# Performance work log

Hardware: AMD Instinct MI355X
Metric: run time of the kernel (lower is better)

## Reference

```python
import jax, jax.numpy as jnp
import numpy as np

N, E, G = 20000, 320000, 128
H, TE, CD = 128, 128, 64
HEADS, DH = 4, 32          # inner = 128 == H
L = 6


def _fwd(p, edge_index, batch):
    """Faithful forward of CrystalDiffusionModel (eval mode: dropout = identity).
    EquivariantGraphConv (imported in the original) is implemented as the standard
    edge-conditioned message-passing conv: m_ij = silu(W[h_src; h_dst; e_ij] + b),
    agg = scatter_add over dst, h' = W_u[h; agg] + b_u."""
    x, ea, t = p['x'], p['edge_attr'], p['t']
    n = x.shape[0]
    h = x @ p['Wn'] + p['bn']                      # [N,H] node embedding
    ef = ea @ p['We'] + p['be']                    # [E,H] edge embedding

    # sinusoidal time embedding -> MLP
    half = TE // 2
    freq = jnp.exp(-jnp.arange(half, dtype=jnp.float32) * (np.log(10000.0) / (half - 1)))
    te = t[:, None] * freq[None, :]
    te = jnp.concatenate([jnp.sin(te), jnp.cos(te)], axis=-1)          # [G,TE]
    te = jax.nn.silu(te @ p['tm_W1'] + p['tm_b1']) @ p['tm_W2'] + p['tm_b2']

    def mlp2(z, W1, b1, W2, b2):
        return jax.nn.silu(z @ W1 + b1) @ W2 + b2

    topo_e = mlp2(p['topo_cond'], p['topo_W1'], p['topo_b1'], p['topo_W2'], p['topo_b2'])
    stab_e = mlp2(p['stab_cond'], p['stab_W1'], p['stab_b1'], p['stab_W2'], p['stab_b2'])
    sust_e = mlp2(p['sust_cond'], p['sust_W1'], p['sust_b1'], p['sust_W2'], p['sust_b2'])
    cond = mlp2(jnp.concatenate([topo_e, stab_e, sust_e], axis=-1),
                p['comb_W1'], p['comb_b1'], p['comb_W2'], p['comb_b2'])  # [G,CD]

    ctx = cond[batch]                               # [N,CD] per-node condition
    # context is a single token per query -> k,v constant across layers
    k = (ctx @ p['Wk']).reshape(n, HEADS, DH)
    v = (ctx @ p['Wv']).reshape(n, HEADS, DH)
    ti = jax.nn.silu(te)[batch]                     # [N,H] time influence (dropout=id)

    src, dst = edge_index[0], edge_index[1]
    scale = DH ** -0.5
    for i in range(L):
        Wm, bm = p['gnn_Wm'][i], p['gnn_bm'][i]
        # split concat-GEMM to avoid materializing [E, 3H]
        m = jax.nn.silu(h[src] @ Wm[:H] + h[dst] @ Wm[H:2 * H] + ef @ Wm[2 * H:] + bm)
        agg = jax.ops.segment_sum(m, dst, num_segments=n)               # [N,H]
        Wu, bu = p['gnn_Wu'][i], p['gnn_bu'][i]
        hu = h @ Wu[:H] + agg @ Wu[H:] + bu
        # LayerNorm
        mu = hu.mean(-1, keepdims=True)
        var = hu.var(-1, keepdims=True)
        hu = (hu - mu) * jax.lax.rsqrt(var + 1e-5) * p['ln_g'][i] + p['ln_b'][i]
        # cross-attention; context length is 1 so softmax over j is exactly 1
        q = (hu @ p['Wq']).reshape(n, HEADS, DH)
        sim = jnp.einsum('nhd,nhd->nh', q, k) * scale                   # [N,heads]
        attn = jax.nn.softmax(sim[..., None], axis=-1)                  # == 1.0
        out = (attn * v).reshape(n, HEADS * DH)
        hu = out @ p['Wo'] + p['bo']
        h = h + hu + ti                              # residual + time influence

    node_pred = jax.nn.silu(h @ p['np_W1'] + p['np_b1']) @ p['np_W2'] + p['np_b2']
    pos_pred = jax.nn.silu(h @ p['pp_W1'] + p['pp_b1']) @ p['pp_W2'] + p['pp_b2']
    return node_pred, pos_pred


def setup_inputs() -> dict:
    key = jax.random.key(0)
    it = iter(jax.random.split(key, 96))

    def nrm(shape, s=0.02):
        return jax.random.normal(next(it), shape, jnp.float32) * s

    z = lambda *s: jnp.zeros(s, jnp.float32)
    inp = {
        'x': jax.random.normal(next(it), (N, 12), jnp.float32),
        'edge_index': jax.random.randint(next(it), (2, E), 0, N),
        'edge_attr': jax.random.normal(next(it), (E, 20), jnp.float32),
        'pos': jax.random.normal(next(it), (N, 3), jnp.float32),
        't': jax.random.uniform(next(it), (G,), jnp.float32) * 1000.0,
        'topo_cond': jax.random.normal(next(it), (G, 7), jnp.float32),
        'stab_cond': jax.random.normal(next(it), (G, 2), jnp.float32),
        'sust_cond': jax.random.normal(next(it), (G, 3), jnp.float32),
        'batch': jnp.sort(jax.random.randint(next(it), (N,), 0, G)),
        'Wn': nrm((12, H)), 'bn': z(H), 'We': nrm((20, H)), 'be': z(H),
        'tm_W1': nrm((TE, 2 * TE)), 'tm_b1': z(2 * TE), 'tm_W2': nrm((2 * TE, TE)), 'tm_b2': z(TE),
        'topo_W1': nrm((7, 32)), 'topo_b1': z(32), 'topo_W2': nrm((32, 32)), 'topo_b2': z(32),
        'stab_W1': nrm((2, 16)), 'stab_b1': z(16), 'stab_W2': nrm((16, 16)), 'stab_b2': z(16),
        'sust_W1': nrm((3, 16)), 'sust_b1': z(16), 'sust_W2': nrm((16, 16)), 'sust_b2': z(16),
        'comb_W1': nrm((64, CD)), 'comb_b1': z(CD), 'comb_W2': nrm((CD, CD)), 'comb_b2': z(CD),
        'Wq': nrm((H, HEADS * DH)), 'Wk': nrm((CD, HEADS * DH)), 'Wv': nrm((CD, HEADS * DH)),
        'Wo': nrm((HEADS * DH, H)), 'bo': z(H),
        'gnn_Wm': nrm((L, 3 * H, H)), 'gnn_bm': z(L, H),
        'gnn_Wu': nrm((L, 2 * H, H)), 'gnn_bu': z(L, H),
        'ln_g': jnp.ones((L, H), jnp.float32), 'ln_b': z(L, H),
        'np_W1': nrm((H, 2 * H)), 'np_b1': z(2 * H), 'np_W2': nrm((2 * H, 12)), 'np_b2': z(12),
        'pp_W1': nrm((H, H)), 'pp_b1': z(H), 'pp_W2': nrm((H, 3)), 'pp_b2': z(3),
    }
    return inp


def reference(x, edge_index, edge_attr, pos, t, topo_cond, stab_cond, sust_cond, batch,
              Wn, bn, We, be, tm_W1, tm_b1, tm_W2, tm_b2,
              topo_W1, topo_b1, topo_W2, topo_b2, stab_W1, stab_b1, stab_W2, stab_b2,
              sust_W1, sust_b1, sust_W2, sust_b2, comb_W1, comb_b1, comb_W2, comb_b2,
              Wq, Wk, Wv, Wo, bo, gnn_Wm, gnn_bm, gnn_Wu, gnn_bu, ln_g, ln_b,
              np_W1, np_b1, np_W2, np_b2, pp_W1, pp_b1, pp_W2, pp_b2):
    loc = dict(locals())
    p = {k: v for k, v in loc.items() if k not in ('edge_index', 'batch', 'pos')}
    return _fwd(p, edge_index, batch)
```

## Files before the change

### kernel.cpp

```cpp
#include <hip/hip_runtime.h>
#include <hip/hip_bf16.h>

#define NN 20000
#define GG 128

typedef __bf16 bf16x8_t __attribute__((ext_vector_type(8)));
typedef float  f32x4_t  __attribute__((ext_vector_type(4)));
typedef __hip_bfloat16 hbf16;

#define PK_NPW1 32768
#define PK_PPW1 65536
#define PK_NPW2 81920
#define PK_PPW2 86016
#define PK_WN   88064

__device__ __forceinline__ float silu_f(float v) {
    return v / (1.0f + expf(-v));
}

__global__ __launch_bounds__(256) void graph_kernel(
        const float* __restrict__ t, const float* __restrict__ topo,
        const float* __restrict__ stab, const float* __restrict__ sust,
        const float* __restrict__ tmW1, const float* __restrict__ tmb1,
        const float* __restrict__ tmW2, const float* __restrict__ tmb2,
        const float* __restrict__ topoW1, const float* __restrict__ topob1,
        const float* __restrict__ topoW2, const float* __restrict__ topob2,
        const float* __restrict__ stabW1, const float* __restrict__ stabb1,
        const float* __restrict__ stabW2, const float* __restrict__ stabb2,
        const float* __restrict__ sustW1, const float* __restrict__ sustb1,
        const float* __restrict__ sustW2, const float* __restrict__ sustb2,
        const float* __restrict__ combW1, const float* __restrict__ combb1,
        const float* __restrict__ combW2, const float* __restrict__ combb2,
        const float* __restrict__ Wv, const float* __restrict__ Wo,
        const float* __restrict__ bo,
        const float* __restrict__ npW1, const float* __restrict__ npW2,
        const float* __restrict__ ppW1, const float* __restrict__ ppW2,
        const float* __restrict__ Wn,
        float* __restrict__ gadd, hbf16* __restrict__ wsb) {
    __shared__ float s_te[128];
    __shared__ float s_th1[256];
    __shared__ float s_tef[128];
    __shared__ float s_l1[64];
    __shared__ float s_cat[64];
    __shared__ float s_c1[64];
    __shared__ float s_cond[64];
    __shared__ float s_v[128];
    __shared__ float s_red[256];

    const int g = blockIdx.x;
    const int tid = threadIdx.x;

    {
#pragma unroll
        for (int e = 0; e < 2; ++e) {
            const int s = blockIdx.x * 512 + e * 256 + tid;
            if (s < 32768) {
                const int p = s;
                const int j = p & 7, l = (p >> 3) & 63, kb = (p >> 9) & 3, ct = p >> 11;
                const int k = kb * 32 + ((l >> 4) << 3) + j;
                const int n = ct * 16 + (l & 15);
                wsb[PK_NPW1 + p] = __float2bfloat16(npW1[k * 256 + n]);
            } else if (s < 49152) {
                const int p = s - 32768;
                const int j = p & 7, l = (p >> 3) & 63, kb = (p >> 9) & 3, ct = p >> 11;
                const int k = kb * 32 + ((l >> 4) << 3) + j;
                const int n = ct * 16 + (l & 15);
                wsb[PK_PPW1 + p] = __float2bfloat16(ppW1[k * 128 + n]);
            } else if (s < 53248) {
                const int p = s - 49152;
                const int j = p & 7, l = (p >> 3) & 63, kb = p >> 9;
                const int k = kb * 32 + ((l >> 4) << 3) + j;
                const int n = l & 15;
                wsb[PK_NPW2 + p] = __float2bfloat16(n < 12 ? npW2[k * 12 + n] : 0.0f);
            } else if (s < 55296) {
                const int p = s - 53248;
                const int j = p & 7, l = (p >> 3) & 63, kb = p >> 9;
                const int k = kb * 32 + ((l >> 4) << 3) + j;
                const int n = l & 15;
                wsb[PK_PPW2 + p] = __float2bfloat16(n < 3 ? ppW2[k * 3 + n] : 0.0f);
            } else if (s < 59392) {
                const int p = s - 55296;
                const int j = p & 7, l = (p >> 3) & 63, ct = p >> 9;
                const int k = ((l >> 4) << 3) + j;
                const int n = ct * 16 + (l & 15);
                wsb[PK_WN + p] = __float2bfloat16(k < 12 ? Wn[k * 128 + n] : 0.0f);
            }
        }
    }

    if (tid < 128) {
        const float tval = t[g];
        const int i = tid & 63;
        const float fr = expf(-(float)i * 0.14619587892025688f);
        const float arg = tval * fr;
        s_te[tid] = (tid < 64) ? sinf(arg) : cosf(arg);
    } else if (tid < 192) {
        const int c = tid - 128;
        if (c < 32) {
            float acc = topob1[c];
            for (int k = 0; k < 7; ++k)
                acc += topo[g * 7 + k] * topoW1[k * 32 + c];
            s_l1[c] = silu_f(acc);
        } else if (c < 48) {
            const int j = c - 32;
            float acc = stabb1[j];
            for (int k = 0; k < 2; ++k)
                acc += stab[g * 2 + k] * stabW1[k * 16 + j];
            s_l1[c] = silu_f(acc);
        } else {
            const int j = c - 48;
            float acc = sustb1[j];
            for (int k = 0; k < 3; ++k)
                acc += sust[g * 3 + k] * sustW1[k * 16 + j];
            s_l1[c] = silu_f(acc);
        }
    }
    __syncthreads();

    {
        float acc = tmb1[tid];
#pragma unroll 4
        for (int k = 0; k < 128; ++k)
            acc += s_te[k] * tmW1[k * 256 + tid];
        s_th1[tid] = silu_f(acc);
    }
    __syncthreads();

    {
        const int j = tid & 127, half = tid >> 7;
        float acc = 0.0f;
#pragma unroll 4
        for (int kk = 0; kk < 128; ++kk)
            acc += s_th1[half * 128 + kk] * tmW2[(half * 128 + kk) * 128 + j];
        s_red[tid] = acc;
    }
    __syncthreads();

    if (tid < 128) {
        s_tef[tid] = tmb2[tid] + s_red[tid] + s_red[tid + 128];
    } else if (tid < 192) {
        const int c = tid - 128;
        if (c < 32) {
            float acc = topob2[c];
            for (int k = 0; k < 32; ++k)
                acc += s_l1[k] * topoW2[k * 32 + c];
            s_cat[c] = acc;
        } else if (c < 48) {
            const int j = c - 32;
            float acc = stabb2[j];
            for (int k = 0; k < 16; ++k)
                acc += s_l1[32 + k] * stabW2[k * 16 + j];
            s_cat[c] = acc;
        } else {
            const int j = c - 48;
            float acc = sustb2[j];
            for (int k = 0; k < 16; ++k)
                acc += s_l1[48 + k] * sustW2[k * 16 + j];
            s_cat[c] = acc;
        }
    }
    __syncthreads();

    {
        const int j = tid & 63, part = tid >> 6;
        float acc = 0.0f;
#pragma unroll
        for (int kk = 0; kk < 16; ++kk)
            acc += s_cat[part * 16 + kk] * combW1[(part * 16 + kk) * 64 + j];
        s_red[tid] = acc;
    }
    __syncthreads();
    if (tid < 64)
        s_c1[tid] = silu_f(combb1[tid] + s_red[tid] + s_red[tid + 64] +
                           s_red[tid + 128] + s_red[tid + 192]);
    __syncthreads();

    {
        const int j = tid & 63, part = tid >> 6;
        float acc = 0.0f;
#pragma unroll
        for (int kk = 0; kk < 16; ++kk)
            acc += s_c1[part * 16 + kk] * combW2[(part * 16 + kk) * 64 + j];
        s_red[tid] = acc;
    }
    __syncthreads();
    if (tid < 64)
        s_cond[tid] = combb2[tid] + s_red[tid] + s_red[tid + 64] +
                      s_red[tid + 128] + s_red[tid + 192];
    __syncthreads();

    {
        const int j = tid & 127, half = tid >> 7;
        float acc = 0.0f;
#pragma unroll
        for (int kk = 0; kk < 32; ++kk)
            acc += s_cond[half * 32 + kk] * Wv[(half * 32 + kk) * 128 + j];
        s_red[tid] = acc;
    }
    __syncthreads();
    if (tid < 128) s_v[tid] = s_red[tid] + s_red[tid + 128];
    __syncthreads();

    {
        const int j = tid & 127, half = tid >> 7;
        float acc = 0.0f;
#pragma unroll 4
        for (int kk = 0; kk < 64; ++kk)
            acc += s_v[half * 64 + kk] * Wo[(half * 64 + kk) * 128 + j];
        s_red[tid] = acc;
    }
    __syncthreads();
    if (tid < 128)
        gadd[g * 128 + tid] =
            6.0f * (bo[tid] + s_red[tid] + s_red[tid + 128] + silu_f(s_tef[tid]));
}

__global__ __launch_bounds__(256, 1) void node_kernel(
        const float* __restrict__ x, const int* __restrict__ batch,
        const float* __restrict__ bn,
        const float* __restrict__ npb1, const float* __restrict__ npb2,
        const float* __restrict__ ppb1, const float* __restrict__ ppb2,
        const float* __restrict__ gadd, const hbf16* __restrict__ wsb,
        float* __restrict__ out) {
    __shared__ __align__(16) hbf16 z1s[4 * 16 * 264];
    __shared__ __align__(16) hbf16 hs[4 * 16 * 136];

    const int tid  = threadIdx.x;
    const int w    = tid >> 6;
    const int lane = tid & 63;
    const int q    = lane >> 4;
    const int r    = lane & 15;
    const int n16  = blockIdx.x * 64 + w * 16;

    hbf16* wz1 = z1s + w * (16 * 264);
    hbf16* wh  = hs  + w * (16 * 136);

    bf16x8_t Ax;
    {
        const int node = n16 + r;
        float xv[8];
#pragma unroll
        for (int j = 0; j < 8; ++j) xv[j] = 0.0f;
        if (node < NN) {
            if (q == 0) {
                const float4 a = *reinterpret_cast<const float4*>(x + node * 12);
                const float4 b = *reinterpret_cast<const float4*>(x + node * 12 + 4);
                xv[0] = a.x; xv[1] = a.y; xv[2] = a.z; xv[3] = a.w;
                xv[4] = b.x; xv[5] = b.y; xv[6] = b.z; xv[7] = b.w;
            } else if (q == 1) {
                const float4 a = *reinterpret_cast<const float4*>(x + node * 12 + 8);
                xv[0] = a.x; xv[1] = a.y; xv[2] = a.z; xv[3] = a.w;
            }
        }
#pragma unroll
        for (int j = 0; j < 8; ++j) {
            const hbf16 tv = __float2bfloat16(xv[j]);
            Ax[j] = *reinterpret_cast<const __bf16*>(&tv);
        }
    }

    int bidx[4];
#pragma unroll
    for (int i = 0; i < 4; ++i) {
        const int gn = n16 + q * 4 + i;
        bidx[i] = (gn < NN) ? batch[gn] : 0;
    }

    f32x4_t hacc[8];
#pragma unroll
    for (int ct = 0; ct < 8; ++ct) {
        const bf16x8_t Bf = *reinterpret_cast<const bf16x8_t*>(
            &wsb[PK_WN + (ct * 64 + lane) * 8]);
        hacc[ct] = __builtin_amdgcn_mfma_f32_16x16x32_bf16(
            Ax, Bf, (f32x4_t){0.f, 0.f, 0.f, 0.f}, 0, 0, 0);
    }
#pragma unroll
    for (int ct = 0; ct < 8; ++ct) {
        const int n = ct * 16 + r;
        const float bv = bn[n];
#pragma unroll
        for (int i = 0; i < 4; ++i) {
            const float hv = hacc[ct][i] + bv + gadd[bidx[i] * 128 + n];
            wh[(q * 4 + i) * 136 + n] = __float2bfloat16(hv);
        }
    }

    bf16x8_t Ah[4];
#pragma unroll
    for (int kb = 0; kb < 4; ++kb)
        Ah[kb] = *reinterpret_cast<const bf16x8_t*>(
            &wh[r * 136 + kb * 32 + q * 8]);

    {
        f32x4_t acc[16];
#pragma unroll
        for (int ct = 0; ct < 16; ++ct) acc[ct] = (f32x4_t){0.f, 0.f, 0.f, 0.f};
#pragma unroll
        for (int kb = 0; kb < 4; ++kb) {
#pragma unroll
            for (int ct = 0; ct < 16; ++ct) {
                const bf16x8_t Bf = *reinterpret_cast<const bf16x8_t*>(
                    &wsb[PK_NPW1 + ((ct * 4 + kb) * 64 + lane) * 8]);
                acc[ct] = __builtin_amdgcn_mfma_f32_16x16x32_bf16(
                    Ah[kb], Bf, acc[ct], 0, 0, 0);
            }
        }
#pragma unroll
        for (int ct = 0; ct < 16; ++ct) {
            const int col = ct * 16 + r;
            const float b1 = npb1[col];
#pragma unroll
            for (int i = 0; i < 4; ++i)
                wz1[(q * 4 + i) * 264 + col] =
                    __float2bfloat16(silu_f(acc[ct][i] + b1));
        }
    }

    {
        f32x4_t acc2 = (f32x4_t){0.f, 0.f, 0.f, 0.f};
#pragma unroll
        for (int kb = 0; kb < 8; ++kb) {
            const bf16x8_t Af = *reinterpret_cast<const bf16x8_t*>(
                &wz1[r * 264 + kb * 32 + q * 8]);
            const bf16x8_t Bf = *reinterpret_cast<const bf16x8_t*>(
                &wsb[PK_NPW2 + (kb * 64 + lane) * 8]);
            acc2 = __builtin_amdgcn_mfma_f32_16x16x32_bf16(Af, Bf, acc2, 0, 0, 0);
        }
        if (r < 12) {
            const float b2 = npb2[r];
#pragma unroll
            for (int i = 0; i < 4; ++i) {
                const int gn = n16 + q * 4 + i;
                if (gn < NN) out[gn * 12 + r] = acc2[i] + b2;
            }
        }
    }

    {
        f32x4_t acc[8];
#pragma unroll
        for (int ct = 0; ct < 8; ++ct) acc[ct] = (f32x4_t){0.f, 0.f, 0.f, 0.f};
#pragma unroll
        for (int kb = 0; kb < 4; ++kb) {
#pragma unroll
            for (int ct = 0; ct < 8; ++ct) {
                const bf16x8_t Bf = *reinterpret_cast<const bf16x8_t*>(
                    &wsb[PK_PPW1 + ((ct * 4 + kb) * 64 + lane) * 8]);
                acc[ct] = __builtin_amdgcn_mfma_f32_16x16x32_bf16(
                    Ah[kb], Bf, acc[ct], 0, 0, 0);
            }
        }
#pragma unroll
        for (int ct = 0; ct < 8; ++ct) {
            const int col = ct * 16 + r;
            const float b1 = ppb1[col];
#pragma unroll
            for (int i = 0; i < 4; ++i)
                wh[(q * 4 + i) * 136 + col] =
                    __float2bfloat16(silu_f(acc[ct][i] + b1));
        }
    }

    {
        f32x4_t acc2 = (f32x4_t){0.f, 0.f, 0.f, 0.f};
#pragma unroll
        for (int kb = 0; kb < 4; ++kb) {
            const bf16x8_t Af = *reinterpret_cast<const bf16x8_t*>(
                &wh[r * 136 + kb * 32 + q * 8]);
            const bf16x8_t Bf = *reinterpret_cast<const bf16x8_t*>(
                &wsb[PK_PPW2 + (kb * 64 + lane) * 8]);
            acc2 = __builtin_amdgcn_mfma_f32_16x16x32_bf16(Af, Bf, acc2, 0, 0, 0);
        }
        if (r < 3) {
            const float b2 = ppb2[r];
#pragma unroll
            for (int i = 0; i < 4; ++i) {
                const int gn = n16 + q * 4 + i;
                if (gn < NN) out[NN * 12 + gn * 3 + r] = acc2[i] + b2;
            }
        }
    }
}

extern "C" void kernel_launch(void* const* d_in, const int* in_sizes, int n_in,
                              void* d_out, int out_size, void* d_ws, size_t ws_size,
                              hipStream_t stream) {
    const float* x      = (const float*)d_in[0];
    const float* t      = (const float*)d_in[4];
    const float* topo   = (const float*)d_in[5];
    const float* stab   = (const float*)d_in[6];
    const float* sust   = (const float*)d_in[7];
    const int*   batch  = (const int*)d_in[8];
    const float* Wn     = (const float*)d_in[9];
    const float* bn     = (const float*)d_in[10];
    const float* tmW1   = (const float*)d_in[13];
    const float* tmb1   = (const float*)d_in[14];
    const float* tmW2   = (const float*)d_in[15];
    const float* tmb2   = (const float*)d_in[16];
    const float* topoW1 = (const float*)d_in[17];
    const float* topob1 = (const float*)d_in[18];
    const float* topoW2 = (const float*)d_in[19];
    const float* topob2 = (const float*)d_in[20];
    const float* stabW1 = (const float*)d_in[21];
    const float* stabb1 = (const float*)d_in[22];
    const float* stabW2 = (const float*)d_in[23];
    const float* stabb2 = (const float*)d_in[24];
    const float* sustW1 = (const float*)d_in[25];
    const float* sustb1 = (const float*)d_in[26];
    const float* sustW2 = (const float*)d_in[27];
    const float* sustb2 = (const float*)d_in[28];
    const float* combW1 = (const float*)d_in[29];
    const float* combb1 = (const float*)d_in[30];
    const float* combW2 = (const float*)d_in[31];
    const float* combb2 = (const float*)d_in[32];
    const float* Wv     = (const float*)d_in[35];
    const float* Wo     = (const float*)d_in[36];
    const float* bo     = (const float*)d_in[37];
    const float* npW1   = (const float*)d_in[44];
    const float* npb1   = (const float*)d_in[45];
    const float* npW2   = (const float*)d_in[46];
    const float* npb2   = (const float*)d_in[47];
    const float* ppW1   = (const float*)d_in[48];
    const float* ppb1   = (const float*)d_in[49];
    const float* ppW2   = (const float*)d_in[50];
    const float* ppb2   = (const float*)d_in[51];

    float* gadd = (float*)d_ws;
    hbf16* wsb  = (hbf16*)d_ws;
    float* out  = (float*)d_out;

    graph_kernel<<<GG, 256, 0, stream>>>(t, topo, stab, sust,
                                         tmW1, tmb1, tmW2, tmb2,
                                         topoW1, topob1, topoW2, topob2,
                                         stabW1, stabb1, stabW2, stabb2,
                                         sustW1, sustb1, sustW2, sustb2,
                                         combW1, combb1, combW2, combb2,
                                         Wv, Wo, bo,
                                         npW1, npW2, ppW1, ppW2, Wn,
                                         gadd, wsb);

    node_kernel<<<(NN + 63) / 64, 256, 0, stream>>>(
        x, batch, bn, npb1, npb2, ppb1, ppb2, gadd, wsb, out);
}
```

Measured before the change: 232.6 us.

## Fuse per-graph conditioning MLPs into node kernel, split weight packing

Moves weight packing into a separate small pack kernel and fuses the per-graph time/condition MLP chain into the node kernel. Each node block recomputes the graph-level additive term for the (up to 4) graphs its 64 nodes span and keeps it in shared memory, so the gadd round trip through global memory is gone. The work is redundant: every graph's MLP is recomputed by several blocks, each block's serial prologue gets longer, and the clamp to 4 graphs per block assumes sorted batches with enough nodes per graph. The z1 and h shared buffers are merged into one to offset the added shared-memory use.

Measured after the change: 255.2 us. +9.7%, slower.

```diff
diff --git a/kernel.cpp b/kernel.cpp
--- a/kernel.cpp
+++ b/kernel.cpp
@@ -8,17 +8,56 @@
 typedef float  f32x4_t  __attribute__((ext_vector_type(4)));
 typedef __hip_bfloat16 hbf16;
 
-#define PK_NPW1 32768
-#define PK_PPW1 65536
-#define PK_NPW2 81920
-#define PK_PPW2 86016
-#define PK_WN   88064
+#define PK_NPW1 0
+#define PK_PPW1 32768
+#define PK_NPW2 49152
+#define PK_PPW2 53248
+#define PK_WN   55296
 
 __device__ __forceinline__ float silu_f(float v) {
     return v / (1.0f + expf(-v));
 }
 
-__global__ __launch_bounds__(256) void graph_kernel(
+__global__ __launch_bounds__(256) void pack_kernel(
+        const float* __restrict__ npW1, const float* __restrict__ npW2,
+        const float* __restrict__ ppW1, const float* __restrict__ ppW2,
+        const float* __restrict__ Wn, hbf16* __restrict__ wsb) {
+    const int s = blockIdx.x * 256 + threadIdx.x;
+    if (s < 32768) {
+        const int p = s;
+        const int j = p & 7, l = (p >> 3) & 63, kb = (p >> 9) & 3, ct = p >> 11;
+        const int k = kb * 32 + ((l >> 4) << 3) + j;
+        const int n = ct * 16 + (l & 15);
+        wsb[PK_NPW1 + p] = __float2bfloat16(npW1[k * 256 + n]);
+    } else if (s < 49152) {
+        const int p = s - 32768;
+        const int j = p & 7, l = (p >> 3) & 63, kb = (p >> 9) & 3, ct = p >> 11;
+        const int k = kb * 32 + ((l >> 4) << 3) + j;
+        const int n = ct * 16 + (l & 15);
+        wsb[PK_PPW1 + p] = __float2bfloat16(ppW1[k * 128 + n]);
+    } else if (s < 53248) {
+        const int p = s - 49152;
+        const int j = p & 7, l = (p >> 3) & 63, kb = p >> 9;
+        const int k = kb * 32 + ((l >> 4) << 3) + j;
+        const int n = l & 15;
+        wsb[PK_NPW2 + p] = __float2bfloat16(n < 12 ? npW2[k * 12 + n] : 0.0f);
+    } else if (s < 55296) {
+        const int p = s - 53248;
+        const int j = p & 7, l = (p >> 3) & 63, kb = p >> 9;
+        const int k = kb * 32 + ((l >> 4) << 3) + j;
+        const int n = l & 15;
+        wsb[PK_PPW2 + p] = __float2bfloat16(n < 3 ? ppW2[k * 3 + n] : 0.0f);
+    } else {
+        const int p = s - 55296;
+        const int j = p & 7, l = (p >> 3) & 63, ct = p >> 9;
+        const int k = ((l >> 4) << 3) + j;
+        const int n = ct * 16 + (l & 15);
+        wsb[PK_WN + p] = __float2bfloat16(k < 12 ? Wn[k * 128 + n] : 0.0f);
+    }
+}
+
+__global__ __launch_bounds__(256) void fused_kernel(
+        const float* __restrict__ x, const int* __restrict__ batch,
         const float* __restrict__ t, const float* __restrict__ topo,
         const float* __restrict__ stab, const float* __restrict__ sust,
         const float* __restrict__ tmW1, const float* __restrict__ tmb1,
@@ -32,11 +71,11 @@
         const float* __restrict__ combW1, const float* __restrict__ combb1,
         const float* __restrict__ combW2, const float* __restrict__ combb2,
         const float* __restrict__ Wv, const float* __restrict__ Wo,
-        const float* __restrict__ bo,
-        const float* __restrict__ npW1, const float* __restrict__ npW2,
-        const float* __restrict__ ppW1, const float* __restrict__ ppW2,
-        const float* __restrict__ Wn,
-        float* __restrict__ gadd, hbf16* __restrict__ wsb) {
+        const float* __restrict__ bo, const float* __restrict__ bn,
+        const float* __restrict__ npb1, const float* __restrict__ npb2,
+        const float* __restrict__ ppb1, const float* __restrict__ ppb2,
+        const hbf16* __restrict__ wsb,
+        float* __restrict__ out) {
     __shared__ float s_te[128];
     __shared__ float s_th1[256];
     __shared__ float s_tef[128];
@@ -46,194 +85,156 @@
     __shared__ float s_cond[64];
     __shared__ float s_v[128];
     __shared__ float s_red[256];
-
-    const int g = blockIdx.x;
+    __shared__ float s_gadd[4][128];
+    __shared__ __align__(16) hbf16 tbuf[4 * 16 * 264];
+
     const int tid = threadIdx.x;
-
-    {
-#pragma unroll
-        for (int e = 0; e < 2; ++e) {
-            const int s = blockIdx.x * 512 + e * 256 + tid;
-            if (s < 32768) {
-                const int p = s;
-                const int j = p & 7, l = (p >> 3) & 63, kb = (p >> 9) & 3, ct = p >> 11;
-                const int k = kb * 32 + ((l >> 4) << 3) + j;
-                const int n = ct * 16 + (l & 15);
-                wsb[PK_NPW1 + p] = __float2bfloat16(npW1[k * 256 + n]);
-            } else if (s < 49152) {
-                const int p = s - 32768;
-                const int j = p & 7, l = (p >> 3) & 63, kb = (p >> 9) & 3, ct = p >> 11;
-                const int k = kb * 32 + ((l >> 4) << 3) + j;
-                const int n = ct * 16 + (l & 15);
-                wsb[PK_PPW1 + p] = __float2bfloat16(ppW1[k * 128 + n]);
-            } else if (s < 53248) {
-                const int p = s - 49152;
-                const int j = p & 7, l = (p >> 3) & 63, kb = p >> 9;
-                const int k = kb * 32 + ((l >> 4) << 3) + j;
-                const int n = l & 15;
-                wsb[PK_NPW2 + p] = __float2bfloat16(n < 12 ? npW2[k * 12 + n] : 0.0f);
-            } else if (s < 55296) {
-                const int p = s - 53248;
-                const int j = p & 7, l = (p >> 3) & 63, kb = p >> 9;
-                const int k = kb * 32 + ((l >> 4) << 3) + j;
-                const int n = l & 15;
-                wsb[PK_PPW2 + p] = __float2bfloat16(n < 3 ? ppW2[k * 3 + n] : 0.0f);
-            } else if (s < 59392) {
-                const int p = s - 55296;
-                const int j = p & 7, l = (p >> 3) & 63, ct = p >> 9;
-                const int k = ((l >> 4) << 3) + j;
-                const int n = ct * 16 + (l & 15);
-                wsb[PK_WN + p] = __float2bfloat16(k < 12 ? Wn[k * 128 + n] : 0.0f);
-            }
-        }
-    }
-
-    if (tid < 128) {
-        const float tval = t[g];
-        const int i = tid & 63;
-        const float fr = expf(-(float)i * 0.14619587892025688f);
-        const float arg = tval * fr;
-        s_te[tid] = (tid < 64) ? sinf(arg) : cosf(arg);
-    } else if (tid < 192) {
-        const int c = tid - 128;
-        if (c < 32) {
-            float acc = topob1[c];
-            for (int k = 0; k < 7; ++k)
-                acc += topo[g * 7 + k] * topoW1[k * 32 + c];
-            s_l1[c] = silu_f(acc);
-        } else if (c < 48) {
-            const int j = c - 32;
-            float acc = stabb1[j];
-            for (int k = 0; k < 2; ++k)
-                acc += stab[g * 2 + k] * stabW1[k * 16 + j];
-            s_l1[c] = silu_f(acc);
-        } else {
-            const int j = c - 48;
-            float acc = sustb1[j];
-            for (int k = 0; k < 3; ++k)
-                acc += sust[g * 3 + k] * sustW1[k * 16 + j];
-            s_l1[c] = silu_f(acc);
-        }
-    }
-    __syncthreads();
-
-    {
-        float acc = tmb1[tid];
+    const int nb = blockIdx.x * 64;
+    const int nlast = (nb + 63 < NN) ? nb + 63 : NN - 1;
+
+    const int g0 = batch[nb];
+    const int g1 = batch[nlast];
+    int ng = g1 - g0 + 1;
+    if (ng > 4) ng = 4;
+
+    for (int gi = 0; gi < ng; ++gi) {
+        const int g = g0 + gi;
+
+        if (tid < 128) {
+            const float tval = t[g];
+            const int i = tid & 63;
+            const float fr = expf(-(float)i * 0.14619587892025688f);
+            const float arg = tval * fr;
+            s_te[tid] = (tid < 64) ? sinf(arg) : cosf(arg);
+        } else if (tid < 192) {
+            const int c = tid - 128;
+            if (c < 32) {
+                float acc = topob1[c];
+                for (int k = 0; k < 7; ++k)
+                    acc += topo[g * 7 + k] * topoW1[k * 32 + c];
+                s_l1[c] = silu_f(acc);
+            } else if (c < 48) {
+                const int j = c - 32;
+                float acc = stabb1[j];
+                for (int k = 0; k < 2; ++k)
+                    acc += stab[g * 2 + k] * stabW1[k * 16 + j];
+                s_l1[c] = silu_f(acc);
+            } else {
+                const int j = c - 48;
+                float acc = sustb1[j];
+                for (int k = 0; k < 3; ++k)
+                    acc += sust[g * 3 + k] * sustW1[k * 16 + j];
+                s_l1[c] = silu_f(acc);
+            }
+        }
+        __syncthreads();
+
+        {
+            float acc = tmb1[tid];
 #pragma unroll 4
-        for (int k = 0; k < 128; ++k)
-            acc += s_te[k] * tmW1[k * 256 + tid];
-        s_th1[tid] = silu_f(acc);
-    }
-    __syncthreads();
-
-    {
-        const int j = tid & 127, half = tid >> 7;
-        float acc = 0.0f;
+            for (int k = 0; k < 128; ++k)
+                acc += s_te[k] * tmW1[k * 256 + tid];
+            s_th1[tid] = silu_f(acc);
+        }
+        __syncthreads();
+
+        {
+            const int j = tid & 127, half = tid >> 7;
+            float acc = 0.0f;
 #pragma unroll 4
-        for (int kk = 0; kk < 128; ++kk)
-            acc += s_th1[half * 128 + kk] * tmW2[(half * 128 + kk) * 128 + j];
-        s_red[tid] = acc;
-    }
-    __syncthreads();
-
-    if (tid < 128) {
-        s_tef[tid] = tmb2[tid] + s_red[tid] + s_red[tid + 128];
-    } else if (tid < 192) {
-        const int c = tid - 128;
-        if (c < 32) {
-            float acc = topob2[c];
-            for (int k = 0; k < 32; ++k)
-                acc += s_l1[k] * topoW2[k * 32 + c];
-            s_cat[c] = acc;
-        } else if (c < 48) {
-            const int j = c - 32;
-            float acc = stabb2[j];
-            for (int k = 0; k < 16; ++k)
-                acc += s_l1[32 + k] * stabW2[k * 16 + j];
-            s_cat[c] = acc;
-        } else {
-            const int j = c - 48;
-            float acc = sustb2[j];
-            for (int k = 0; k < 16; ++k)
-                acc += s_l1[48 + k] * sustW2[k * 16 + j];
-            s_cat[c] = acc;
-        }
-    }
-    __syncthreads();
-
-    {
-        const int j = tid & 63, part = tid >> 6;
-        float acc = 0.0f;
-#pragma unroll
-        for (int kk = 0; kk < 16; ++kk)
-            acc += s_cat[part * 16 + kk] * combW1[(part * 16 + kk) * 64 + j];
-        s_red[tid] = acc;
-    }
-    __syncthreads();
-    if (tid < 64)
-        s_c1[tid] = silu_f(combb1[tid] + s_red[tid] + s_red[tid + 64] +
-                           s_red[tid + 128] + s_red[tid + 192]);
-    __syncthreads();
-
-    {
-        const int j = tid & 63, part = tid >> 6;
-        float acc = 0.0f;
-#pragma unroll
-        for (int kk = 0; kk < 16; ++kk)
-            acc += s_c1[part * 16 + kk] * combW2[(part * 16 + kk) * 64 + j];
-        s_red[tid] = acc;
-    }
-    __syncthreads();
-    if (tid < 64)
-        s_cond[tid] = combb2[tid] + s_red[tid] + s_red[tid + 64] +
-                      s_red[tid + 128] + s_red[tid + 192];
-    __syncthreads();
-
-    {
-        const int j = tid & 127, half = tid >> 7;
-        float acc = 0.0f;
-#pragma unroll
-        for (int kk = 0; kk < 32; ++kk)
-            acc += s_cond[half * 32 + kk] * Wv[(half * 32 + kk) * 128 + j];
-        s_red[tid] = acc;
-    }
-    __syncthreads();
-    if (tid < 128) s_v[tid] = s_red[tid] + s_red[tid + 128];
-    __syncthreads();
-
-    {
-        const int j = tid & 127, half = tid >> 7;
-        float acc = 0.0f;
+            for (int kk = 0; kk < 128; ++kk)
+                acc += s_th1[half * 128 + kk] * tmW2[(half * 128 + kk) * 128 + j];
+            s_red[tid] = acc;
+        }
+        __syncthreads();
+
+        if (tid < 128) {
+            s_tef[tid] = tmb2[tid] + s_red[tid] + s_red[tid + 128];
+        } else if (tid < 192) {
+            const int c = tid - 128;
+            if (c < 32) {
+                float acc = topob2[c];
+                for (int k = 0; k < 32; ++k)
+                    acc += s_l1[k] * topoW2[k * 32 + c];
+                s_cat[c] = acc;
+            } else if (c < 48) {
+                const int j = c - 32;
+                float acc = stabb2[j];
+                for (int k = 0; k < 16; ++k)
+                    acc += s_l1[32 + k] * stabW2[k * 16 + j];
+                s_cat[c] = acc;
+            } else {
+                const int j = c - 48;
+                float acc = sustb2[j];
+                for (int k = 0; k < 16; ++k)
+                    acc += s_l1[48 + k] * sustW2[k * 16 + j];
+                s_cat[c] = acc;
+            }
+        }
+        __syncthreads();
+
+        {
+            const int j = tid & 63, part = tid >> 6;
+            float acc = 0.0f;
+#pragma unroll
+            for (int kk = 0; kk < 16; ++kk)
+                acc += s_cat[part * 16 + kk] * combW1[(part * 16 + kk) * 64 + j];
+            s_red[tid] = acc;
+        }
+        __syncthreads();
+        if (tid < 64)
+            s_c1[tid] = silu_f(combb1[tid] + s_red[tid] + s_red[tid + 64] +
+                               s_red[tid + 128] + s_red[tid + 192]);
+        __syncthreads();
+
+        {
+            const int j = tid & 63, part = tid >> 6;
+            float acc = 0.0f;
+#pragma unroll
+            for (int kk = 0; kk < 16; ++kk)
+                acc += s_c1[part * 16 + kk] * combW2[(part * 16 + kk) * 64 + j];
+            s_red[tid] = acc;
+        }
+        __syncthreads();
+        if (tid < 64)
+            s_cond[tid] = combb2[tid] + s_red[tid] + s_red[tid + 64] +
+                          s_red[tid + 128] + s_red[tid + 192];
+        __syncthreads();
+
+        {
+            const int j = tid & 127, half = tid >> 7;
+            float acc = 0.0f;
+#pragma unroll
+            for (int kk = 0; kk < 32; ++kk)
+                acc += s_cond[half * 32 + kk] * Wv[(half * 32 + kk) * 128 + j];
+            s_red[tid] = acc;
+        }
+        __syncthreads();
+        if (tid < 128) s_v[tid] = s_red[tid] + s_red[tid + 128];
+        __syncthreads();
+
+        {
+            const int j = tid & 127, half = tid >> 7;
+            float acc = 0.0f;
 #pragma unroll 4
-        for (int kk = 0; kk < 64; ++kk)
-            acc += s_v[half * 64 + kk] * Wo[(half * 64 + kk) * 128 + j];
-        s_red[tid] = acc;
-    }
-    __syncthreads();
-    if (tid < 128)
-        gadd[g * 128 + tid] =
-            6.0f * (bo[tid] + s_red[tid] + s_red[tid + 128] + silu_f(s_tef[tid]));
-}
-
-__global__ __launch_bounds__(256, 1) void node_kernel(
-        const float* __restrict__ x, const int* __restrict__ batch,
-        const float* __restrict__ bn,
-        const float* __restrict__ npb1, const float* __restrict__ npb2,
-        const float* __restrict__ ppb1, const float* __restrict__ ppb2,
-        const float* __restrict__ gadd, const hbf16* __restrict__ wsb,
-        float* __restrict__ out) {
-    __shared__ __align__(16) hbf16 z1s[4 * 16 * 264];
-    __shared__ __align__(16) hbf16 hs[4 * 16 * 136];
-
-    const int tid  = threadIdx.x;
+            for (int kk = 0; kk < 64; ++kk)
+                acc += s_v[half * 64 + kk] * Wo[(half * 64 + kk) * 128 + j];
+            s_red[tid] = acc;
+        }
+        __syncthreads();
+        if (tid < 128)
+            s_gadd[gi][tid] =
+                6.0f * (bo[tid] + s_red[tid] + s_red[tid + 128] + silu_f(s_tef[tid]));
+        __syncthreads();
+    }
+
     const int w    = tid >> 6;
     const int lane = tid & 63;
     const int q    = lane >> 4;
     const int r    = lane & 15;
-    const int n16  = blockIdx.x * 64 + w * 16;
-
-    hbf16* wz1 = z1s + w * (16 * 264);
-    hbf16* wh  = hs  + w * (16 * 136);
+    const int n16  = nb + w * 16;
+
+    hbf16* wb = tbuf + w * (16 * 264);
 
     bf16x8_t Ax;
     {
@@ -259,29 +260,35 @@
         }
     }
 
-    int bidx[4];
+    int gidx[4];
 #pragma unroll
     for (int i = 0; i < 4; ++i) {
         const int gn = n16 + q * 4 + i;
-        bidx[i] = (gn < NN) ? batch[gn] : 0;
-    }
-
-    f32x4_t hacc[8];
-#pragma unroll
-    for (int ct = 0; ct < 8; ++ct) {
-        const bf16x8_t Bf = *reinterpret_cast<const bf16x8_t*>(
-            &wsb[PK_WN + (ct * 64 + lane) * 8]);
-        hacc[ct] = __builtin_amdgcn_mfma_f32_16x16x32_bf16(
-            Ax, Bf, (f32x4_t){0.f, 0.f, 0.f, 0.f}, 0, 0, 0);
-    }
-#pragma unroll
-    for (int ct = 0; ct < 8; ++ct) {
-        const int n = ct * 16 + r;
-        const float bv = bn[n];
-#pragma unroll
-        for (int i = 0; i < 4; ++i) {
-            const float hv = hacc[ct][i] + bv + gadd[bidx[i] * 128 + n];
-            wh[(q * 4 + i) * 136 + n] = __float2bfloat16(hv);
+        int b = (gn < NN) ? batch[gn] : g0;
+        int d = b - g0;
+        if (d < 0) d = 0;
+        if (d > ng - 1) d = ng - 1;
+        gidx[i] = d;
+    }
+
+    {
+        f32x4_t hacc[8];
+#pragma unroll
+        for (int ct = 0; ct < 8; ++ct) {
+            const bf16x8_t Bf = *reinterpret_cast<const bf16x8_t*>(
+                &wsb[PK_WN + (ct * 64 + lane) * 8]);
+            hacc[ct] = __builtin_amdgcn_mfma_f32_16x16x32_bf16(
+                Ax, Bf, (f32x4_t){0.f, 0.f, 0.f, 0.f}, 0, 0, 0);
+        }
+#pragma unroll
+        for (int ct = 0; ct < 8; ++ct) {
+            const int n = ct * 16 + r;
+            const float bv = bn[n];
+#pragma unroll
+            for (int i = 0; i < 4; ++i) {
+                const float hv = hacc[ct][i] + bv + s_gadd[gidx[i]][n];
+                wb[(q * 4 + i) * 136 + n] = __float2bfloat16(hv);
+            }
         }
     }
 
@@ -289,7 +296,7 @@
 #pragma unroll
     for (int kb = 0; kb < 4; ++kb)
         Ah[kb] = *reinterpret_cast<const bf16x8_t*>(
-            &wh[r * 136 + kb * 32 + q * 8]);
+            &wb[r * 136 + kb * 32 + q * 8]);
 
     {
         f32x4_t acc[16];
@@ -311,7 +318,7 @@
             const float b1 = npb1[col];
 #pragma unroll
             for (int i = 0; i < 4; ++i)
-                wz1[(q * 4 + i) * 264 + col] =
+                wb[(q * 4 + i) * 264 + col] =
                     __float2bfloat16(silu_f(acc[ct][i] + b1));
         }
     }
@@ -321,7 +328,7 @@
 #pragma unroll
         for (int kb = 0; kb < 8; ++kb) {
             const bf16x8_t Af = *reinterpret_cast<const bf16x8_t*>(
-                &wz1[r * 264 + kb * 32 + q * 8]);
+                &wb[r * 264 + kb * 32 + q * 8]);
             const bf16x8_t Bf = *reinterpret_cast<const bf16x8_t*>(
                 &wsb[PK_NPW2 + (kb * 64 + lane) * 8]);
             acc2 = __builtin_amdgcn_mfma_f32_16x16x32_bf16(Af, Bf, acc2, 0, 0, 0);
@@ -356,7 +363,7 @@
             const float b1 = ppb1[col];
 #pragma unroll
             for (int i = 0; i < 4; ++i)
-                wh[(q * 4 + i) * 136 + col] =
+                wb[(q * 4 + i) * 136 + col] =
                     __float2bfloat16(silu_f(acc[ct][i] + b1));
         }
     }
@@ -366,7 +373,7 @@
 #pragma unroll
         for (int kb = 0; kb < 4; ++kb) {
             const bf16x8_t Af = *reinterpret_cast<const bf16x8_t*>(
-                &wh[r * 136 + kb * 32 + q * 8]);
+                &wb[r * 136 + kb * 32 + q * 8]);
             const bf16x8_t Bf = *reinterpret_cast<const bf16x8_t*>(
                 &wsb[PK_PPW2 + (kb * 64 + lane) * 8]);
             acc2 = __builtin_amdgcn_mfma_f32_16x16x32_bf16(Af, Bf, acc2, 0, 0, 0);
@@ -425,20 +432,18 @@
     const float* ppW2   = (const float*)d_in[50];
     const float* ppb2   = (const float*)d_in[51];
 
-    float* gadd = (float*)d_ws;
-    hbf16* wsb  = (hbf16*)d_ws;
-    float* out  = (float*)d_out;
-
-    graph_kernel<<<GG, 256, 0, stream>>>(t, topo, stab, sust,
-                                         tmW1, tmb1, tmW2, tmb2,
-                                         topoW1, topob1, topoW2, topob2,
-                                         stabW1, stabb1, stabW2, stabb2,
-                                         sustW1, sustb1, sustW2, sustb2,
-                                         combW1, combb1, combW2, combb2,
-                                         Wv, Wo, bo,
-                                         npW1, npW2, ppW1, ppW2, Wn,
-                                         gadd, wsb);
-
-    node_kernel<<<(NN + 63) / 64, 256, 0, stream>>>(
-        x, batch, bn, npb1, npb2, ppb1, ppb2, gadd, wsb, out);
+    hbf16* wsb = (hbf16*)d_ws;
+    float* out = (float*)d_out;
+
+    pack_kernel<<<232, 256, 0, stream>>>(npW1, npW2, ppW1, ppW2, Wn, wsb);
+
+    fused_kernel<<<(NN + 63) / 64, 256, 0, stream>>>(
+        x, batch, t, topo, stab, sust,
+        tmW1, tmb1, tmW2, tmb2,
+        topoW1, topob1, topoW2, topob2,
+        stabW1, stabb1, stabW2, stabb2,
+        sustW1, sustb1, sustW2, sustb2,
+        combW1, combb1, combW2, combb2,
+        Wv, Wo, bo, bn, npb1, npb2, ppb1, ppb2,
+        wsb, out);
 }
```

## Stage packed weights and biases in LDS, split weight packing into extra blocks

Applied to the files above, without the earlier changes.

The node kernel now stages each packed bf16 weight matrix chunk into shared memory, along with the biases, the batch indices and a window of per-graph additive vectors. Previously every wave read the weight fragments straight from global memory. The weight packing is moved into separate extra blocks of the prep kernel, so the per-graph MLP blocks no longer do it. Smaller per-wave register footprints, the dropped single-block launch bound, fast exp/rcp in silu and larger unroll factors aim for higher occupancy and less global traffic. The cost is many more __syncthreads barriers between chunk loads.

After: 203.0 us. 1.15x faster.

```diff
diff --git a/kernel.cpp b/kernel.cpp
--- a/kernel.cpp
+++ b/kernel.cpp
@@ -8,17 +8,18 @@
 typedef float  f32x4_t  __attribute__((ext_vector_type(4)));
 typedef __hip_bfloat16 hbf16;
 
-#define PK_NPW1 32768
-#define PK_PPW1 65536
-#define PK_NPW2 81920
-#define PK_PPW2 86016
-#define PK_WN   88064
+#define PK_NPW1 0
+#define PK_PPW1 32768
+#define PK_NPW2 49152
+#define PK_PPW2 53248
+#define PK_WN   55296
+#define GADD_OFF 59392
 
 __device__ __forceinline__ float silu_f(float v) {
-    return v / (1.0f + expf(-v));
+    return v * __builtin_amdgcn_rcpf(1.0f + __expf(-v));
 }
 
-__global__ __launch_bounds__(256) void graph_kernel(
+__global__ __launch_bounds__(256) void prep_kernel(
         const float* __restrict__ t, const float* __restrict__ topo,
         const float* __restrict__ stab, const float* __restrict__ sust,
         const float* __restrict__ tmW1, const float* __restrict__ tmb1,
@@ -37,6 +38,44 @@
         const float* __restrict__ ppW1, const float* __restrict__ ppW2,
         const float* __restrict__ Wn,
         float* __restrict__ gadd, hbf16* __restrict__ wsb) {
+    const int tid = threadIdx.x;
+
+    if (blockIdx.x >= GG) {
+        const int s = (blockIdx.x - GG) * 256 + tid;
+        if (s < 32768) {
+            const int p = s;
+            const int j = p & 7, l = (p >> 3) & 63, kb = (p >> 9) & 3, ct = p >> 11;
+            const int k = kb * 32 + ((l >> 4) << 3) + j;
+            const int n = ct * 16 + (l & 15);
+            wsb[PK_NPW1 + p] = __float2bfloat16(npW1[k * 256 + n]);
+        } else if (s < 49152) {
+            const int p = s - 32768;
+            const int j = p & 7, l = (p >> 3) & 63, kb = (p >> 9) & 3, ct = p >> 11;
+            const int k = kb * 32 + ((l >> 4) << 3) + j;
+            const int n = ct * 16 + (l & 15);
+            wsb[PK_PPW1 + p] = __float2bfloat16(ppW1[k * 128 + n]);
+        } else if (s < 53248) {
+            const int p = s - 49152;
+            const int j = p & 7, l = (p >> 3) & 63, kb = p >> 9;
+            const int k = kb * 32 + ((l >> 4) << 3) + j;
+            const int n = l & 15;
+            wsb[PK_NPW2 + p] = __float2bfloat16(n < 12 ? npW2[k * 12 + n] : 0.0f);
+        } else if (s < 55296) {
+            const int p = s - 53248;
+            const int j = p & 7, l = (p >> 3) & 63, kb = p >> 9;
+            const int k = kb * 32 + ((l >> 4) << 3) + j;
+            const int n = l & 15;
+            wsb[PK_PPW2 + p] = __float2bfloat16(n < 3 ? ppW2[k * 3 + n] : 0.0f);
+        } else if (s < 59392) {
+            const int p = s - 55296;
+            const int j = p & 7, l = (p >> 3) & 63, ct = p >> 9;
+            const int k = ((l >> 4) << 3) + j;
+            const int n = ct * 16 + (l & 15);
+            wsb[PK_WN + p] = __float2bfloat16(k < 12 ? Wn[k * 128 + n] : 0.0f);
+        }
+        return;
+    }
+
     __shared__ float s_te[128];
     __shared__ float s_th1[256];
     __shared__ float s_tef[128];
@@ -48,50 +87,11 @@
     __shared__ float s_red[256];
 
     const int g = blockIdx.x;
-    const int tid = threadIdx.x;
-
-    {
-#pragma unroll
-        for (int e = 0; e < 2; ++e) {
-            const int s = blockIdx.x * 512 + e * 256 + tid;
-            if (s < 32768) {
-                const int p = s;
-                const int j = p & 7, l = (p >> 3) & 63, kb = (p >> 9) & 3, ct = p >> 11;
-                const int k = kb * 32 + ((l >> 4) << 3) + j;
-                const int n = ct * 16 + (l & 15);
-                wsb[PK_NPW1 + p] = __float2bfloat16(npW1[k * 256 + n]);
-            } else if (s < 49152) {
-                const int p = s - 32768;
-                const int j = p & 7, l = (p >> 3) & 63, kb = (p >> 9) & 3, ct = p >> 11;
-                const int k = kb * 32 + ((l >> 4) << 3) + j;
-                const int n = ct * 16 + (l & 15);
-                wsb[PK_PPW1 + p] = __float2bfloat16(ppW1[k * 128 + n]);
-            } else if (s < 53248) {
-                const int p = s - 49152;
-                const int j = p & 7, l = (p >> 3) & 63, kb = p >> 9;
-                const int k = kb * 32 + ((l >> 4) << 3) + j;
-                const int n = l & 15;
-                wsb[PK_NPW2 + p] = __float2bfloat16(n < 12 ? npW2[k * 12 + n] : 0.0f);
-            } else if (s < 55296) {
-                const int p = s - 53248;
-                const int j = p & 7, l = (p >> 3) & 63, kb = p >> 9;
-                const int k = kb * 32 + ((l >> 4) << 3) + j;
-                const int n = l & 15;
-                wsb[PK_PPW2 + p] = __float2bfloat16(n < 3 ? ppW2[k * 3 + n] : 0.0f);
-            } else if (s < 59392) {
-                const int p = s - 55296;
-                const int j = p & 7, l = (p >> 3) & 63, ct = p >> 9;
-                const int k = ((l >> 4) << 3) + j;
-                const int n = ct * 16 + (l & 15);
-                wsb[PK_WN + p] = __float2bfloat16(k < 12 ? Wn[k * 128 + n] : 0.0f);
-            }
-        }
-    }
 
     if (tid < 128) {
         const float tval = t[g];
         const int i = tid & 63;
-        const float fr = expf(-(float)i * 0.14619587892025688f);
+        const float fr = __expf(-(float)i * 0.14619587892025688f);
         const float arg = tval * fr;
         s_te[tid] = (tid < 64) ? sinf(arg) : cosf(arg);
     } else if (tid < 192) {
@@ -119,7 +119,7 @@
 
     {
         float acc = tmb1[tid];
-#pragma unroll 4
+#pragma unroll 16
         for (int k = 0; k < 128; ++k)
             acc += s_te[k] * tmW1[k * 256 + tid];
         s_th1[tid] = silu_f(acc);
@@ -129,7 +129,7 @@
     {
         const int j = tid & 127, half = tid >> 7;
         float acc = 0.0f;
-#pragma unroll 4
+#pragma unroll 16
         for (int kk = 0; kk < 128; ++kk)
             acc += s_th1[half * 128 + kk] * tmW2[(half * 128 + kk) * 128 + j];
         s_red[tid] = acc;
@@ -192,7 +192,7 @@
     {
         const int j = tid & 127, half = tid >> 7;
         float acc = 0.0f;
-#pragma unroll
+#pragma unroll 16
         for (int kk = 0; kk < 32; ++kk)
             acc += s_cond[half * 32 + kk] * Wv[(half * 32 + kk) * 128 + j];
         s_red[tid] = acc;
@@ -204,7 +204,7 @@
     {
         const int j = tid & 127, half = tid >> 7;
         float acc = 0.0f;
-#pragma unroll 4
+#pragma unroll 16
         for (int kk = 0; kk < 64; ++kk)
             acc += s_v[half * 64 + kk] * Wo[(half * 64 + kk) * 128 + j];
         s_red[tid] = acc;
@@ -215,25 +215,64 @@
             6.0f * (bo[tid] + s_red[tid] + s_red[tid + 128] + silu_f(s_tef[tid]));
 }
 
-__global__ __launch_bounds__(256, 1) void node_kernel(
+#define NGS 8
+
+__global__ __launch_bounds__(256) void node_kernel(
         const float* __restrict__ x, const int* __restrict__ batch,
         const float* __restrict__ bn,
         const float* __restrict__ npb1, const float* __restrict__ npb2,
         const float* __restrict__ ppb1, const float* __restrict__ ppb2,
         const float* __restrict__ gadd, const hbf16* __restrict__ wsb,
         float* __restrict__ out) {
-    __shared__ __align__(16) hbf16 z1s[4 * 16 * 264];
-    __shared__ __align__(16) hbf16 hs[4 * 16 * 136];
+    __shared__ __align__(16) hbf16 s_w[8192];
+    __shared__ __align__(16) hbf16 tbuf[4 * 16 * 264];
+    __shared__ float s_gadd[NGS * 128];
+    __shared__ float s_bias[528];
+    __shared__ int   s_bi[64];
 
     const int tid  = threadIdx.x;
+    const int nb   = blockIdx.x * 64;
     const int w    = tid >> 6;
     const int lane = tid & 63;
     const int q    = lane >> 4;
     const int r    = lane & 15;
-    const int n16  = blockIdx.x * 64 + w * 16;
-
-    hbf16* wz1 = z1s + w * (16 * 264);
-    hbf16* wh  = hs  + w * (16 * 136);
+    const int n16  = nb + w * 16;
+
+    hbf16* wb = tbuf + w * (16 * 264);
+
+    if (tid < 64) {
+        int gn = nb + tid;
+        if (gn > NN - 1) gn = NN - 1;
+        s_bi[tid] = batch[gn];
+    }
+    {
+        int i = tid;
+        if (i < 128) s_bias[i] = bn[i];
+        else if (i < 384) s_bias[i] = npb1[i - 128];
+        else if (i < 396) s_bias[i] = npb2[i - 384];
+        else if (i < 524) s_bias[i] = ppb1[i - 396];
+        else if (i < 527) s_bias[i] = ppb2[i - 524];
+        i = tid + 256;
+        if (i < 384) s_bias[i] = npb1[i - 128];
+        else if (i < 396) s_bias[i] = npb2[i - 384];
+        else if (i < 524) s_bias[i] = ppb1[i - 396];
+        else if (i < 527) s_bias[i] = ppb2[i - 524];
+    }
+    {
+        const uint4* src = reinterpret_cast<const uint4*>(wsb + PK_WN);
+        uint4* dst = reinterpret_cast<uint4*>(s_w);
+        for (int i = tid; i < 512; i += 256) dst[i] = src[i];
+    }
+    __syncthreads();
+
+    const int g0 = s_bi[0];
+    {
+        for (int i = tid; i < NGS * 128; i += 256) {
+            int gr = g0 + (i >> 7);
+            if (gr > GG - 1) gr = GG - 1;
+            s_gadd[i] = gadd[gr * 128 + (i & 127)];
+        }
+    }
 
     bf16x8_t Ax;
     {
@@ -258,30 +297,30 @@
             Ax[j] = *reinterpret_cast<const __bf16*>(&tv);
         }
     }
-
-    int bidx[4];
-#pragma unroll
-    for (int i = 0; i < 4; ++i) {
-        const int gn = n16 + q * 4 + i;
-        bidx[i] = (gn < NN) ? batch[gn] : 0;
-    }
-
-    f32x4_t hacc[8];
-#pragma unroll
-    for (int ct = 0; ct < 8; ++ct) {
-        const bf16x8_t Bf = *reinterpret_cast<const bf16x8_t*>(
-            &wsb[PK_WN + (ct * 64 + lane) * 8]);
-        hacc[ct] = __builtin_amdgcn_mfma_f32_16x16x32_bf16(
-            Ax, Bf, (f32x4_t){0.f, 0.f, 0.f, 0.f}, 0, 0, 0);
-    }
-#pragma unroll
-    for (int ct = 0; ct < 8; ++ct) {
-        const int n = ct * 16 + r;
-        const float bv = bn[n];
-#pragma unroll
-        for (int i = 0; i < 4; ++i) {
-            const float hv = hacc[ct][i] + bv + gadd[bidx[i] * 128 + n];
-            wh[(q * 4 + i) * 136 + n] = __float2bfloat16(hv);
+    __syncthreads();
+
+    {
+        f32x4_t hacc[8];
+#pragma unroll
+        for (int ct = 0; ct < 8; ++ct) {
+            const bf16x8_t Bf = *reinterpret_cast<const bf16x8_t*>(
+                &s_w[(ct * 64 + lane) * 8]);
+            hacc[ct] = __builtin_amdgcn_mfma_f32_16x16x32_bf16(
+                Ax, Bf, (f32x4_t){0.f, 0.f, 0.f, 0.f}, 0, 0, 0);
+        }
+#pragma unroll
+        for (int ct = 0; ct < 8; ++ct) {
+            const int n = ct * 16 + r;
+            const float bv = s_bias[n];
+#pragma unroll
+            for (int i = 0; i < 4; ++i) {
+                const int nl = w * 16 + q * 4 + i;
+                const int gi = s_bi[nl] - g0;
+                float ga;
+                if (gi < NGS) ga = s_gadd[gi * 128 + n];
+                else          ga = gadd[(g0 + gi) * 128 + n];
+                wb[(q * 4 + i) * 136 + n] = __float2bfloat16(hacc[ct][i] + bv + ga);
+            }
         }
     }
 
@@ -289,45 +328,53 @@
 #pragma unroll
     for (int kb = 0; kb < 4; ++kb)
         Ah[kb] = *reinterpret_cast<const bf16x8_t*>(
-            &wh[r * 136 + kb * 32 + q * 8]);
-
-    {
-        f32x4_t acc[16];
-#pragma unroll
-        for (int ct = 0; ct < 16; ++ct) acc[ct] = (f32x4_t){0.f, 0.f, 0.f, 0.f};
-#pragma unroll
-        for (int kb = 0; kb < 4; ++kb) {
-#pragma unroll
-            for (int ct = 0; ct < 16; ++ct) {
+            &wb[r * 136 + kb * 32 + q * 8]);
+
+    for (int c = 0; c < 4; ++c) {
+        __syncthreads();
+        {
+            const uint4* src = reinterpret_cast<const uint4*>(wsb + PK_NPW1 + c * 8192);
+            uint4* dst = reinterpret_cast<uint4*>(s_w);
+            for (int i = tid; i < 1024; i += 256) dst[i] = src[i];
+        }
+        __syncthreads();
+#pragma unroll
+        for (int ci = 0; ci < 4; ++ci) {
+            f32x4_t acc = (f32x4_t){0.f, 0.f, 0.f, 0.f};
+#pragma unroll
+            for (int kb = 0; kb < 4; ++kb) {
                 const bf16x8_t Bf = *reinterpret_cast<const bf16x8_t*>(
-                    &wsb[PK_NPW1 + ((ct * 4 + kb) * 64 + lane) * 8]);
-                acc[ct] = __builtin_amdgcn_mfma_f32_16x16x32_bf16(
-                    Ah[kb], Bf, acc[ct], 0, 0, 0);
+                    &s_w[((ci * 4 + kb) * 64 + lane) * 8]);
+                acc = __builtin_amdgcn_mfma_f32_16x16x32_bf16(Ah[kb], Bf, acc, 0, 0, 0);
             }
-        }
-#pragma unroll
-        for (int ct = 0; ct < 16; ++ct) {
+            const int ct = c * 4 + ci;
             const int col = ct * 16 + r;
-            const float b1 = npb1[col];
+            const float b1 = s_bias[128 + col];
 #pragma unroll
             for (int i = 0; i < 4; ++i)
-                wz1[(q * 4 + i) * 264 + col] =
-                    __float2bfloat16(silu_f(acc[ct][i] + b1));
-        }
-    }
-
+                wb[(q * 4 + i) * 264 + col] = __float2bfloat16(silu_f(acc[i] + b1));
+        }
+    }
+
+    __syncthreads();
+    {
+        const uint4* src = reinterpret_cast<const uint4*>(wsb + PK_NPW2);
+        uint4* dst = reinterpret_cast<uint4*>(s_w);
+        for (int i = tid; i < 512; i += 256) dst[i] = src[i];
+    }
+    __syncthreads();
     {
         f32x4_t acc2 = (f32x4_t){0.f, 0.f, 0.f, 0.f};
 #pragma unroll
         for (int kb = 0; kb < 8; ++kb) {
             const bf16x8_t Af = *reinterpret_cast<const bf16x8_t*>(
-                &wz1[r * 264 + kb * 32 + q * 8]);
+                &wb[r * 264 + kb * 32 + q * 8]);
             const bf16x8_t Bf = *reinterpret_cast<const bf16x8_t*>(
-                &wsb[PK_NPW2 + (kb * 64 + lane) * 8]);
+                &s_w[(kb * 64 + lane) * 8]);
             acc2 = __builtin_amdgcn_mfma_f32_16x16x32_bf16(Af, Bf, acc2, 0, 0, 0);
         }
         if (r < 12) {
-            const float b2 = npb2[r];
+            const float b2 = s_bias[384 + r];
 #pragma unroll
             for (int i = 0; i < 4; ++i) {
                 const int gn = n16 + q * 4 + i;
@@ -336,43 +383,51 @@
         }
     }
 
-    {
-        f32x4_t acc[8];
-#pragma unroll
-        for (int ct = 0; ct < 8; ++ct) acc[ct] = (f32x4_t){0.f, 0.f, 0.f, 0.f};
-#pragma unroll
-        for (int kb = 0; kb < 4; ++kb) {
-#pragma unroll
-            for (int ct = 0; ct < 8; ++ct) {
+    for (int c = 0; c < 2; ++c) {
+        __syncthreads();
+        {
+            const uint4* src = reinterpret_cast<const uint4*>(wsb + PK_PPW1 + c * 8192);
+            uint4* dst = reinterpret_cast<uint4*>(s_w);
+            for (int i = tid; i < 1024; i += 256) dst[i] = src[i];
+        }
+        __syncthreads();
+#pragma unroll
+        for (int ci = 0; ci < 4; ++ci) {
+            f32x4_t acc = (f32x4_t){0.f, 0.f, 0.f, 0.f};
+#pragma unroll
+            for (int kb = 0; kb < 4; ++kb) {
                 const bf16x8_t Bf = *reinterpret_cast<const bf16x8_t*>(
-                    &wsb[PK_PPW1 + ((ct * 4 + kb) * 64 + lane) * 8]);
-                acc[ct] = __builtin_amdgcn_mfma_f32_16x16x32_bf16(
-                    Ah[kb], Bf, acc[ct], 0, 0, 0);
+                    &s_w[((ci * 4 + kb) * 64 + lane) * 8]);
+                acc = __builtin_amdgcn_mfma_f32_16x16x32_bf16(Ah[kb], Bf, acc, 0, 0, 0);
             }
-        }
-#pragma unroll
-        for (int ct = 0; ct < 8; ++ct) {
+            const int ct = c * 4 + ci;
             const int col = ct * 16 + r;
-            const float b1 = ppb1[col];
+            const float b1 = s_bias[396 + col];
 #pragma unroll
             for (int i = 0; i < 4; ++i)
-                wh[(q * 4 + i) * 136 + col] =
-                    __float2bfloat16(silu_f(acc[ct][i] + b1));
-        }
-    }
-
+                wb[(q * 4 + i) * 136 + col] = __float2bfloat16(silu_f(acc[i] + b1));
+        }
+    }
+
+    __syncthreads();
+    {
+        const uint4* src = reinterpret_cast<const uint4*>(wsb + PK_PPW2);
+        uint4* dst = reinterpret_cast<uint4*>(s_w);
+        for (int i = tid; i < 256; i += 256) dst[i] = src[i];
+    }
+    __syncthreads();
     {
         f32x4_t acc2 = (f32x4_t){0.f, 0.f, 0.f, 0.f};
 #pragma unroll
         for (int kb = 0; kb < 4; ++kb) {
             const bf16x8_t Af = *reinterpret_cast<const bf16x8_t*>(
-                &wh[r * 136 + kb * 32 + q * 8]);
+                &wb[r * 136 + kb * 32 + q * 8]);
             const bf16x8_t Bf = *reinterpret_cast<const bf16x8_t*>(
-                &wsb[PK_PPW2 + (kb * 64 + lane) * 8]);
+                &s_w[(kb * 64 + lane) * 8]);
             acc2 = __builtin_amdgcn_mfma_f32_16x16x32_bf16(Af, Bf, acc2, 0, 0, 0);
         }
         if (r < 3) {
-            const float b2 = ppb2[r];
+            const float b2 = s_bias[524 + r];
 #pragma unroll
             for (int i = 0; i < 4; ++i) {
                 const int gn = n16 + q * 4 + i;
@@ -425,19 +480,20 @@
     const float* ppW2   = (const float*)d_in[50];
     const float* ppb2   = (const float*)d_in[51];
 
-    float* gadd = (float*)d_ws;
-    hbf16* wsb  = (hbf16*)d_ws;
-    float* out  = (float*)d_out;
-
-    graph_kernel<<<GG, 256, 0, stream>>>(t, topo, stab, sust,
-                                         tmW1, tmb1, tmW2, tmb2,
-                                         topoW1, topob1, topoW2, topob2,
-                                         stabW1, stabb1, stabW2, stabb2,
-                                         sustW1, sustb1, sustW2, sustb2,
-                                         combW1, combb1, combW2, combb2,
-                                         Wv, Wo, bo,
-                                         npW1, npW2, ppW1, ppW2, Wn,
-                                         gadd, wsb);
+    hbf16* wsb = (hbf16*)d_ws;
+    float* gadd = (float*)(wsb + GADD_OFF);
+    float* out = (float*)d_out;
+
+    prep_kernel<<<GG + 232, 256, 0, stream>>>(
+        t, topo, stab, sust,
+        tmW1, tmb1, tmW2, tmb2,
+        topoW1, topob1, topoW2, topob2,
+        stabW1, stabb1, stabW2, stabb2,
+        sustW1, sustb1, sustW2, sustb2,
+        combW1, combb1, combW2, combb2,
+        Wv, Wo, bo,
+        npW1, npW2, ppW1, ppW2, Wn,
+        gadd, wsb);
 
     node_kernel<<<(NN + 63) / 64, 256, 0, stream>>>(
         x, batch, bn, npb1, npb2, ppb1, ppb2, gadd, wsb, out);
```
